# Optimization experiments

Hardware: AMD Instinct MI355X
Metric: run time of the kernel (lower is better)

The kernel has to match this reference:

```python
import jax, jax.numpy as jnp
import numpy as np

N = 50000      # total nodes
E = 800000     # total edges (before self-loops)
B = 512        # graphs in batch
H = 4          # attention heads
D = 64         # per-head dim (hidden 256 = H*D)
F_IN = 203     # node feature dim
HID = H * D
NEG_SLOPE = 0.2  # PyG GATConv LeakyReLU default
LN_EPS = 1e-5


def setup_inputs() -> dict:
    key = jax.random.key(0)
    ks = jax.random.split(key, 24)
    g = lambda k, shape, fan: (jax.random.normal(k, shape, jnp.float32) / np.sqrt(fan))
    inp = {
        "x": jax.random.normal(ks[0], (N, F_IN), jnp.float32),
        "edge_index": jax.random.randint(ks[1], (2, E), 0, N, jnp.int64),
        "edge_weight": jax.random.uniform(ks[2], (E,), jnp.float32),
        "batch": jnp.sort(jax.random.randint(ks[3], (N,), 0, B, jnp.int64)),
        # GAT layer 1 params
        "W1": g(ks[4], (HID, F_IN), F_IN),
        "a_s1": g(ks[5], (H, D), D),
        "a_d1": g(ks[6], (H, D), D),
        "a_e1": g(ks[7], (H, D), D),
        "We1": g(ks[8], (HID, 1), 1),
        "b1": jnp.zeros((HID,), jnp.float32),
        # GAT layer 2 params
        "W2": g(ks[9], (HID, HID), HID),
        "a_s2": g(ks[10], (H, D), D),
        "a_d2": g(ks[11], (H, D), D),
        "a_e2": g(ks[12], (H, D), D),
        "We2": g(ks[13], (HID, 1), 1),
        "b2": jnp.zeros((HID,), jnp.float32),
        # LayerNorms
        "ln1_g": jnp.ones((HID,), jnp.float32),
        "ln1_b": jnp.zeros((HID,), jnp.float32),
        "ln2_g": jnp.ones((HID,), jnp.float32),
        "ln2_b": jnp.zeros((HID,), jnp.float32),
    }
    return inp


def _gat(x, src, dst, e_attr, W, a_s, a_d, a_e, We, bias, n_nodes):
    # projected node features: [N, H, D]
    xp = (x @ W.T).reshape(n_nodes, H, D)
    alpha_src = jnp.einsum('nhd,hd->nh', xp, a_s)   # [N, H]
    alpha_dst = jnp.einsum('nhd,hd->nh', xp, a_d)   # [N, H]
    ep = (e_attr @ We.T).reshape(-1, H, D)          # [E', H, D]
    alpha_edge = jnp.einsum('ehd,hd->eh', ep, a_e)  # [E', H]
    logits = jax.nn.leaky_relu(alpha_src[src] + alpha_dst[dst] + alpha_edge, NEG_SLOPE)
    # segment softmax over incoming edges per destination node
    m = jax.ops.segment_max(logits, dst, num_segments=n_nodes)
    ex = jnp.exp(logits - m[dst])
    denom = jax.ops.segment_sum(ex, dst, num_segments=n_nodes)
    alpha = ex / denom[dst]                          # [E', H]
    msg = alpha[:, :, None] * xp[src]                # [E', H, D]
    out = jax.ops.segment_sum(msg, dst, num_segments=n_nodes)
    return out.reshape(n_nodes, HID) + bias


def _ln(x, g, b):
    mu = x.mean(-1, keepdims=True)
    var = ((x - mu) ** 2).mean(-1, keepdims=True)
    return (x - mu) * jax.lax.rsqrt(var + LN_EPS) * g + b


def reference(x, edge_index, edge_weight, batch,
              W1, a_s1, a_d1, a_e1, We1, b1,
              W2, a_s2, a_d2, a_e2, We2, b2,
              ln1_g, ln1_b, ln2_g, ln2_b):
    n = x.shape[0]
    # PyG GATConv add_self_loops=True, edge_attr fill_value='mean'
    loop = jnp.arange(n)
    src = jnp.concatenate([edge_index[0], loop])
    dst = jnp.concatenate([edge_index[1], loop])
    ew = jnp.concatenate([edge_weight, jnp.full((n,), edge_weight.mean(), edge_weight.dtype)])
    e_attr = ew[:, None]  # edge_dim = 1

    h = _gat(x, src, dst, e_attr, W1, a_s1, a_d1, a_e1, We1, b1, n)
    h = jax.nn.elu(_ln(h, ln1_g, ln1_b))  # dropout omitted (eval mode)
    h = _gat(h, src, dst, e_attr, W2, a_s2, a_d2, a_e2, We2, b2, n)
    h = jax.nn.elu(_ln(h, ln2_g, ln2_b))

    # global_mean_pool
    s = jax.ops.segment_sum(h, batch, num_segments=B)
    cnt = jax.ops.segment_sum(jnp.ones((n,), h.dtype), batch, num_segments=B)
    return s / jnp.maximum(cnt, 1.0)[:, None]
```

## Files before the change

### kernel.cpp

```cpp
#include <hip/hip_runtime.h>
#include <math.h>

#define HID 256
#define NEG_SLOPE 0.2f
#define LN_EPS 1e-5f

typedef __attribute__((ext_vector_type(4))) float f32x4;
typedef __attribute__((ext_vector_type(8))) short bf16x8;
typedef __attribute__((address_space(3))) unsigned char lds_b;
typedef const __attribute__((address_space(1))) unsigned char glob_b;

__device__ __forceinline__ float bf2f_lo(unsigned int u) {
    union { unsigned int i; float f; } c; c.i = u << 16; return c.f;
}
__device__ __forceinline__ float bf2f_hi(unsigned int u) {
    union { unsigned int i; float f; } c; c.i = u & 0xffff0000u; return c.f;
}
__device__ __forceinline__ float bf2f_u(unsigned short u) {
    union { unsigned int i; float f; } c; c.i = ((unsigned int)u) << 16; return c.f;
}
__device__ __forceinline__ unsigned short f2bf(float f) {
    union { float f; unsigned int i; } c; c.f = f;
    unsigned int i = c.i;
    return (unsigned short)((i + 0x7fffu + ((i >> 16) & 1u)) >> 16);
}

__global__ __launch_bounds__(256) void k_sum_hist(const float* __restrict__ ew, int E,
                                                  const int* __restrict__ ei, int N,
                                                  float* __restrict__ partials, int* __restrict__ deg) {
    int t = threadIdx.x;
    if (blockIdx.x < 256) {
        __shared__ float sdata[4];
        float v = 0.f;
        for (int i = blockIdx.x * 256 + t; i < E; i += 65536) v += ew[i];
        for (int o = 32; o; o >>= 1) v += __shfl_xor(v, o);
        if ((t & 63) == 0) sdata[t >> 6] = v;
        __syncthreads();
        if (t == 0) partials[blockIdx.x] = sdata[0] + sdata[1] + sdata[2] + sdata[3];
    } else {
        int e = (blockIdx.x - 256) * 256 + t;
        if (e >= E + N) return;
        int d = (e < E) ? ei[E + e] : (e - E);
        atomicAdd(&deg[d], 1);
    }
}

__global__ __launch_bounds__(256) void k_scanred_coeff(const int* __restrict__ deg, int N, int NB,
                                                       int* __restrict__ bsum,
                                                       const float* __restrict__ partials, float* __restrict__ sumw,
                                                       const float* __restrict__ We1, const float* __restrict__ ae1,
                                                       const float* __restrict__ We2, const float* __restrict__ ae2,
                                                       float* __restrict__ c1, float* __restrict__ c2) {
    int t = threadIdx.x;
    int b = blockIdx.x;
    if (b < NB) {
        __shared__ int sdata[4];
        int i = b * 256 + t;
        int v = (i < N) ? deg[i] : 0;
        for (int o = 32; o; o >>= 1) v += __shfl_xor(v, o);
        if ((t & 63) == 0) sdata[t >> 6] = v;
        __syncthreads();
        if (t == 0) bsum[b] = sdata[0] + sdata[1] + sdata[2] + sdata[3];
    } else if (b == NB) {
        __shared__ float sdata[4];
        float v = partials[t];
        for (int o = 32; o; o >>= 1) v += __shfl_xor(v, o);
        if ((t & 63) == 0) sdata[t >> 6] = v;
        __syncthreads();
        if (t == 0) *sumw = sdata[0] + sdata[1] + sdata[2] + sdata[3];
    } else {
        float v1 = We1[t] * ae1[t];
        float v2 = We2[t] * ae2[t];
        for (int o = 1; o < 64; o <<= 1) { v1 += __shfl_xor(v1, o); v2 += __shfl_xor(v2, o); }
        if ((t & 63) == 0) { c1[t >> 6] = v1; c2[t >> 6] = v2; }
    }
}

__global__ __launch_bounds__(256) void k_scan_apply(const int* __restrict__ deg, int N, int NB,
                                                    const int* __restrict__ bsum,
                                                    int* __restrict__ offs, int* __restrict__ cursor) {
    __shared__ int sm[256];
    __shared__ int sb[256];
    int t = threadIdx.x;
    int i = blockIdx.x * 256 + t;
    int v = (i < N) ? deg[i] : 0;
    int vb = (t < NB) ? bsum[t] : 0;
    sm[t] = v;
    sb[t] = vb;
    __syncthreads();
    for (int o = 1; o < 256; o <<= 1) {
        int tv = (t >= o) ? sm[t - o] : 0;
        int tb = (t >= o) ? sb[t - o] : 0;
        __syncthreads();
        sm[t] += tv;
        sb[t] += tb;
        __syncthreads();
    }
    int myb = bsum[blockIdx.x];
    int boff = sb[blockIdx.x] - myb;
    if (i < N) {
        int e = boff + sm[t] - v;
        offs[i] = e; cursor[i] = e;
        if (i == N - 1) offs[N] = boff + sm[t];
    }
}

__global__ __launch_bounds__(256) void k_scatter_cvt(const int* __restrict__ ei, int E, int N, int NS,
                                                     int* __restrict__ cursor, int* __restrict__ csr_eid,
                                                     const float* __restrict__ W1, const float* __restrict__ W2,
                                                     unsigned short* __restrict__ o1, unsigned short* __restrict__ o2, int K1,
                                                     const float* __restrict__ x, unsigned short* __restrict__ x16, int FIN) {
    int t = threadIdx.x;
    int b = blockIdx.x;
    if (b < NS) {
        int e = b * 256 + t;
        if (e >= E + N) return;
        int d = (e < E) ? ei[E + e] : (e - E);
        int pos = atomicAdd(&cursor[d], 1);
        csr_eid[pos] = e;
    } else if (b < NS + 512) {
        int wb = b - NS;
        const float* in = (wb < 256) ? W1 : W2;
        unsigned short* out = (wb < 256) ? o1 : o2;
        int K = (wb < 256) ? K1 : 256;
        int col = wb & 255;
        float v = (t < K) ? in[(size_t)col * K + t] : 0.f;
        int ks = t >> 5, j = (t >> 3) & 3, e = t & 7;
        out[ks * 8192 + j * 2048 + ((((col << 4) ^ (j << 4))) >> 1) + e] = f2bf(v);
    } else {
        int r = b - NS - 512;
        x16[(size_t)r * 256 + t] = (t < FIN) ? f2bf(x[(size_t)r * FIN + t]) : (unsigned short)0;
    }
}

__device__ __forceinline__ void gemm_dev(int bid,
    const unsigned short* __restrict__ A16, const unsigned short* __restrict__ Bt16, int M,
    const float* __restrict__ asf, const float* __restrict__ adf,
    unsigned short* __restrict__ C16, float* __restrict__ as_out, float* __restrict__ ad_out)
{
    __shared__ __align__(16) unsigned short Bsl[4 * 256 * 8];
    int t = threadIdx.x;
    int lane = t & 63, w = t >> 6;
    int row0 = bid << 5;
    int kg = lane >> 4, fr = lane & 15;

    int ar0 = row0 + fr;      if (ar0 >= M) ar0 = 0;
    int ar1 = row0 + 16 + fr; if (ar1 >= M) ar1 = 0;
    const unsigned short* ap0 = A16 + (size_t)ar0 * 256 + (kg << 3);
    const unsigned short* ap1 = A16 + (size_t)ar1 * 256 + (kg << 3);

    f32x4 acc[2][4];
#pragma unroll
    for (int i = 0; i < 2; i++)
#pragma unroll
        for (int j = 0; j < 4; j++) acc[i][j] = (f32x4){0.f, 0.f, 0.f, 0.f};

    for (int ks = 0; ks < 8; ks++) {
#pragma unroll
        for (int j = 0; j < 4; j++) {
            __builtin_amdgcn_global_load_lds(
                (glob_b*)(Bt16 + (size_t)ks * 8192 + j * 2048 + t * 8),
                (lds_b*)((char*)Bsl + j * 4096 + t * 16),
                16, 0, 0);
        }
        bf16x8 a0 = *(const bf16x8*)(ap0 + (ks << 5));
        bf16x8 a1 = *(const bf16x8*)(ap1 + (ks << 5));
        __syncthreads();
#pragma unroll
        for (int nf = 0; nf < 4; nf++) {
            int col = (w << 6) + (nf << 4) + fr;
            bf16x8 bv = *(const bf16x8*)((const char*)Bsl + (kg << 12) + (((col << 4)) ^ (kg << 4)));
            acc[0][nf] = __builtin_amdgcn_mfma_f32_16x16x32_bf16(a0, bv, acc[0][nf], 0, 0, 0);
            acc[1][nf] = __builtin_amdgcn_mfma_f32_16x16x32_bf16(a1, bv, acc[1][nf], 0, 0, 0);
        }
        __syncthreads();
    }

#pragma unroll
    for (int mf = 0; mf < 2; mf++)
#pragma unroll
        for (int j = 0; j < 4; j++) {
            int gr = row0 + mf * 16 + kg * 4 + j;
            if (gr < M) {
#pragma unroll
                for (int nf = 0; nf < 4; nf++)
                    C16[(size_t)gr * 256 + (w << 6) + (nf << 4) + fr] = f2bf(acc[mf][nf][j]);
            }
        }
    float asv[4], adv[4];
#pragma unroll
    for (int nf = 0; nf < 4; nf++) {
        int col = (w << 6) + (nf << 4) + fr;
        asv[nf] = asf[col]; adv[nf] = adf[col];
    }
#pragma unroll
    for (int mf = 0; mf < 2; mf++)
#pragma unroll
        for (int j = 0; j < 4; j++) {
            float ps = acc[mf][0][j] * asv[0] + acc[mf][1][j] * asv[1] + acc[mf][2][j] * asv[2] + acc[mf][3][j] * asv[3];
            float pd = acc[mf][0][j] * adv[0] + acc[mf][1][j] * adv[1] + acc[mf][2][j] * adv[2] + acc[mf][3][j] * adv[3];
#pragma unroll
            for (int o = 1; o < 16; o <<= 1) { ps += __shfl_xor(ps, o); pd += __shfl_xor(pd, o); }
            if (fr == 0) {
                int gr = row0 + mf * 16 + kg * 4 + j;
                if (gr < M) {
                    as_out[gr * 4 + w] = ps;
                    ad_out[gr * 4 + w] = pd;
                }
            }
        }
}

__device__ __forceinline__ void sort_gather_dev(int bid, const int* __restrict__ offs, int* __restrict__ eid,
                                                const int* __restrict__ ei, const float* __restrict__ ew,
                                                const float* __restrict__ sumw, int E, int N,
                                                int* __restrict__ csr_src, float* __restrict__ csr_w) {
    int lane = threadIdx.x & 63;
    int n = (bid << 2) + (threadIdx.x >> 6);
    if (n >= N) return;
    int s0 = offs[n];
    int d = offs[n + 1] - s0;
    if (d <= 0) return;
    if (d <= 64) {
        int key = (lane < d) ? eid[s0 + lane] : 0x7fffffff;
        int rank = 0;
        for (int j = 0; j < d; j++) {
            int kj = __shfl(key, j);
            rank += (kj < key) ? 1 : 0;
        }
        if (lane < d) {
            int s; float wv;
            if (key < E) { s = ei[key]; wv = ew[key]; }
            else         { s = key - E; wv = *sumw / (float)E; }
            csr_src[s0 + rank] = s;
            csr_w[s0 + rank] = wv;
        }
    } else {
        if (lane == 0) {
            for (int i = s0 + 1; i < s0 + d; i++) {
                int ke = eid[i];
                int j = i - 1;
                while (j >= s0 && eid[j] > ke) { eid[j + 1] = eid[j]; j--; }
                eid[j + 1] = ke;
            }
        }
        __builtin_amdgcn_wave_barrier();
        for (int i = lane; i < d; i += 64) {
            int e = eid[s0 + i];
            int s; float wv;
            if (e < E) { s = ei[e]; wv = ew[e]; }
            else       { s = e - E; wv = *sumw / (float)E; }
            csr_src[s0 + i] = s;
            csr_w[s0 + i] = wv;
        }
    }
}

__global__ __launch_bounds__(256) void k_gemm_sort(int MB,
    const unsigned short* __restrict__ A16, const unsigned short* __restrict__ Bt16, int M,
    const float* __restrict__ asf, const float* __restrict__ adf,
    unsigned short* __restrict__ C16, float* __restrict__ as_out, float* __restrict__ ad_out,
    const int* __restrict__ offs, int* __restrict__ eid,
    const int* __restrict__ ei, const float* __restrict__ ew,
    const float* __restrict__ sumw, int E,
    int* __restrict__ csr_src, float* __restrict__ csr_w) {
    if ((int)blockIdx.x < MB)
        gemm_dev(blockIdx.x, A16, Bt16, M, asf, adf, C16, as_out, ad_out);
    else
        sort_gather_dev(blockIdx.x - MB, offs, eid, ei, ew, sumw, E, M, csr_src, csr_w);
}

__global__ __launch_bounds__(256) void gemm_mfma(
    const unsigned short* __restrict__ A16, const unsigned short* __restrict__ Bt16, int M,
    const float* __restrict__ asf, const float* __restrict__ adf,
    unsigned short* __restrict__ C16, float* __restrict__ as_out, float* __restrict__ ad_out) {
    gemm_dev(blockIdx.x, A16, Bt16, M, asf, adf, C16, as_out, ad_out);
}

#define ACC8(u, q) do { \
    acc0 += (q) * bf2f_lo((u).x); acc1 += (q) * bf2f_hi((u).x); \
    acc2 += (q) * bf2f_lo((u).y); acc3 += (q) * bf2f_hi((u).y); \
    acc4 += (q) * bf2f_lo((u).z); acc5 += (q) * bf2f_hi((u).z); \
    acc6 += (q) * bf2f_lo((u).w); acc7 += (q) * bf2f_hi((u).w); } while (0)

__global__ __launch_bounds__(256) void gat_kernel(
    const unsigned short* __restrict__ xp16, const int* __restrict__ offs,
    const int* __restrict__ csr_src, const float* __restrict__ csr_w,
    const float* __restrict__ as_, const float* __restrict__ ad_,
    const float* __restrict__ cvec, const float* __restrict__ bias,
    const float* __restrict__ ln_g, const float* __restrict__ ln_b,
    int N, unsigned short* __restrict__ out16) {
    __shared__ float p_lds[4][256];
    __shared__ int   s_lds[4][64];
    int lane = threadIdx.x & 63;
    int wid = threadIdx.x >> 6;
    int n = (blockIdx.x << 2) + wid;
    if (n >= N) return;
    int start = offs[n], end = offs[n + 1];
    int e0 = lane >> 5;
    int colb = lane & 31;
    int hq2 = colb >> 3;
    const unsigned short* xbase = xp16 + (size_t)colb * 8;
    float4 adv = *(const float4*)(ad_ + (size_t)n * 4);
    float c0 = cvec[0], c1 = cvec[1], c2 = cvec[2], c3 = cvec[3];
    float m = -INFINITY, dn = 0.f;
    float acc0 = 0, acc1 = 0, acc2 = 0, acc3 = 0, acc4 = 0, acc5 = 0, acc6 = 0, acc7 = 0;

    for (int base = start; base < end; base += 64) {
        int idx = base + lane;
        bool act = idx < end;
        int s = act ? csr_src[idx] : 0;
        float w = act ? csr_w[idx] : 0.f;
        float4 av = *(const float4*)(as_ + (size_t)s * 4);
        float l0 = av.x + adv.x + w * c0; l0 = l0 >= 0.f ? l0 : NEG_SLOPE * l0;
        float l1 = av.y + adv.y + w * c1; l1 = l1 >= 0.f ? l1 : NEG_SLOPE * l1;
        float l2 = av.z + adv.z + w * c2; l2 = l2 >= 0.f ? l2 : NEG_SLOPE * l2;
        float l3 = av.w + adv.w + w * c3; l3 = l3 >= 0.f ? l3 : NEG_SLOPE * l3;
        float lm = fmaxf(fmaxf(l0, l1), fmaxf(l2, l3));
        if (!act) lm = -INFINITY;
        for (int o = 32; o; o >>= 1) lm = fmaxf(lm, __shfl_xor(lm, o));
        float nm = fmaxf(m, lm);
        float sc = __expf(m - nm);
        m = nm;
        dn *= sc;
        acc0 *= sc; acc1 *= sc; acc2 *= sc; acc3 *= sc;
        acc4 *= sc; acc5 *= sc; acc6 *= sc; acc7 *= sc;
        float p0 = act ? __expf(l0 - m) : 0.f;
        float p1 = act ? __expf(l1 - m) : 0.f;
        float p2 = act ? __expf(l2 - m) : 0.f;
        float p3 = act ? __expf(l3 - m) : 0.f;
        float4 pv = { p0, p1, p2, p3 };
        *(float4*)&p_lds[wid][lane << 2] = pv;
        s_lds[wid][lane] = s;
        int cnt = end - base; if (cnt > 64) cnt = 64;
        int k = 0;
        for (; k + 8 <= cnt; k += 8) {
            int i0 = k + e0, i1 = k + 2 + e0, i2 = k + 4 + e0, i3 = k + 6 + e0;
            int s0 = s_lds[wid][i0], s1 = s_lds[wid][i1], s2 = s_lds[wid][i2], s3 = s_lds[wid][i3];
            uint4 u0 = *(const uint4*)(xbase + (size_t)s0 * 256);
            uint4 u1 = *(const uint4*)(xbase + (size_t)s1 * 256);
            uint4 u2 = *(const uint4*)(xbase + (size_t)s2 * 256);
            uint4 u3 = *(const uint4*)(xbase + (size_t)s3 * 256);
            float q0 = p_lds[wid][(i0 << 2) + hq2];
            float q1 = p_lds[wid][(i1 << 2) + hq2];
            float q2 = p_lds[wid][(i2 << 2) + hq2];
            float q3 = p_lds[wid][(i3 << 2) + hq2];
            dn += q0 + q1 + q2 + q3;
            ACC8(u0, q0); ACC8(u1, q1); ACC8(u2, q2); ACC8(u3, q3);
        }
        for (; k < cnt; k += 2) {
            int i = k + e0;
            bool v = i < cnt;
            int si = s_lds[wid][v ? i : 0];
            float qi = v ? p_lds[wid][(i << 2) + hq2] : 0.f;
            uint4 u = *(const uint4*)(xbase + (size_t)si * 256);
            dn += qi;
            ACC8(u, qi);
        }
    }
    acc0 += __shfl_xor(acc0, 32); acc1 += __shfl_xor(acc1, 32);
    acc2 += __shfl_xor(acc2, 32); acc3 += __shfl_xor(acc3, 32);
    acc4 += __shfl_xor(acc4, 32); acc5 += __shfl_xor(acc5, 32);
    acc6 += __shfl_xor(acc6, 32); acc7 += __shfl_xor(acc7, 32);
    dn += __shfl_xor(dn, 32);
    float inv = 1.f / dn;
    int cb8 = colb << 3;
    float4 bA = *(const float4*)(bias + cb8);
    float4 bB = *(const float4*)(bias + cb8 + 4);
    float o0 = acc0 * inv + bA.x, o1 = acc1 * inv + bA.y, o2 = acc2 * inv + bA.z, o3 = acc3 * inv + bA.w;
    float o4 = acc4 * inv + bB.x, o5 = acc5 * inv + bB.y, o6 = acc6 * inv + bB.z, o7 = acc7 * inv + bB.w;
    float part = ((o0 + o1) + (o2 + o3)) + ((o4 + o5) + (o6 + o7));
    for (int o = 16; o; o >>= 1) part += __shfl_xor(part, o);
    float mu = part * (1.f / 256.f);
    float d0 = o0 - mu, d1 = o1 - mu, d2 = o2 - mu, d3 = o3 - mu;
    float d4 = o4 - mu, d5 = o5 - mu, d6 = o6 - mu, d7 = o7 - mu;
    float vpart = ((d0 * d0 + d1 * d1) + (d2 * d2 + d3 * d3)) + ((d4 * d4 + d5 * d5) + (d6 * d6 + d7 * d7));
    for (int o = 16; o; o >>= 1) vpart += __shfl_xor(vpart, o);
    float rstd = rsqrtf(vpart * (1.f / 256.f) + LN_EPS);
    float4 gA = *(const float4*)(ln_g + cb8), gB = *(const float4*)(ln_g + cb8 + 4);
    float4 eA = *(const float4*)(ln_b + cb8), eB = *(const float4*)(ln_b + cb8 + 4);
    float y0 = d0 * rstd * gA.x + eA.x; y0 = y0 > 0.f ? y0 : __expf(y0) - 1.f;
    float y1 = d1 * rstd * gA.y + eA.y; y1 = y1 > 0.f ? y1 : __expf(y1) - 1.f;
    float y2 = d2 * rstd * gA.z + eA.z; y2 = y2 > 0.f ? y2 : __expf(y2) - 1.f;
    float y3 = d3 * rstd * gA.w + eA.w; y3 = y3 > 0.f ? y3 : __expf(y3) - 1.f;
    float y4 = d4 * rstd * gB.x + eB.x; y4 = y4 > 0.f ? y4 : __expf(y4) - 1.f;
    float y5 = d5 * rstd * gB.y + eB.y; y5 = y5 > 0.f ? y5 : __expf(y5) - 1.f;
    float y6 = d6 * rstd * gB.z + eB.z; y6 = y6 > 0.f ? y6 : __expf(y6) - 1.f;
    float y7 = d7 * rstd * gB.w + eB.w; y7 = y7 > 0.f ? y7 : __expf(y7) - 1.f;
    if (lane < 32) {
        uint4 ov;
        ov.x = ((unsigned int)f2bf(y1) << 16) | f2bf(y0);
        ov.y = ((unsigned int)f2bf(y3) << 16) | f2bf(y2);
        ov.z = ((unsigned int)f2bf(y5) << 16) | f2bf(y4);
        ov.w = ((unsigned int)f2bf(y7) << 16) | f2bf(y6);
        *(uint4*)(out16 + (size_t)n * HID + cb8) = ov;
    }
}

__device__ __forceinline__ int lower_bound_i(const int* a, int n, int key) {
    int lo = 0, hi = n;
    while (lo < hi) { int mid = (lo + hi) >> 1; if (a[mid] < key) lo = mid + 1; else hi = mid; }
    return lo;
}

__global__ __launch_bounds__(256) void pool_kernel(const unsigned short* __restrict__ h, const int* __restrict__ batch,
                                                   int N, float* __restrict__ out) {
    int b = blockIdx.x;
    int lo = lower_bound_i(batch, N, b);
    int hi = lower_bound_i(batch, N, b + 1);
    float a0 = 0.f, a1 = 0.f, a2 = 0.f, a3 = 0.f;
    int n = lo;
    for (; n + 4 <= hi; n += 4) {
        a0 += bf2f_u(h[(size_t)(n + 0) * HID + threadIdx.x]);
        a1 += bf2f_u(h[(size_t)(n + 1) * HID + threadIdx.x]);
        a2 += bf2f_u(h[(size_t)(n + 2) * HID + threadIdx.x]);
        a3 += bf2f_u(h[(size_t)(n + 3) * HID + threadIdx.x]);
    }
    for (; n < hi; n++) a0 += bf2f_u(h[(size_t)n * HID + threadIdx.x]);
    float acc = (a0 + a1) + (a2 + a3);
    out[(size_t)b * HID + threadIdx.x] = acc / fmaxf((float)(hi - lo), 1.f);
}

extern "C" void kernel_launch(void* const* d_in, const int* in_sizes, int n_in,
                              void* d_out, int out_size, void* d_ws, size_t ws_size,
                              hipStream_t stream) {
    const float* x    = (const float*)d_in[0];
    const int*   ei   = (const int*)d_in[1];
    const float* ew   = (const float*)d_in[2];
    const int*   batch= (const int*)d_in[3];
    const float* W1   = (const float*)d_in[4];
    const float* as1  = (const float*)d_in[5];
    const float* ad1  = (const float*)d_in[6];
    const float* ae1  = (const float*)d_in[7];
    const float* We1  = (const float*)d_in[8];
    const float* b1   = (const float*)d_in[9];
    const float* W2   = (const float*)d_in[10];
    const float* as2  = (const float*)d_in[11];
    const float* ad2  = (const float*)d_in[12];
    const float* ae2  = (const float*)d_in[13];
    const float* We2  = (const float*)d_in[14];
    const float* b2   = (const float*)d_in[15];
    const float* ln1g = (const float*)d_in[16];
    const float* ln1b = (const float*)d_in[17];
    const float* ln2g = (const float*)d_in[18];
    const float* ln2b = (const float*)d_in[19];

    int N = in_sizes[3];
    int E = in_sizes[2];
    int FIN = in_sizes[0] / N;
    int EN = E + N;
    int B = out_size / HID;
    float* outp = (float*)d_out;
    int NB = (N + 255) / 256;
    int NS = (EN + 255) / 256;

    char* ws = (char*)d_ws;
    size_t off = 0;
    auto alloc = [&](size_t bytes) { void* p = ws + off; off = (off + bytes + 255) & ~(size_t)255; return p; };
    float* sumw    = (float*)alloc(4);
    int*   deg     = (int*)  alloc((size_t)N * 4);
    size_t zero_bytes = 256 + (size_t)N * 4;
    float* partials= (float*)alloc(256 * 4);
    int*   bsum    = (int*)  alloc(256 * 4);
    int*   offs    = (int*)  alloc((size_t)(N + 1) * 4);
    int*   cursor  = (int*)  alloc((size_t)N * 4);
    int*   csr_eid = (int*)  alloc((size_t)EN * 4);
    int*   csr_src = (int*)  alloc((size_t)EN * 4);
    float* csr_w   = (float*)alloc((size_t)EN * 4);
    float* asb     = (float*)alloc((size_t)N * 4 * 4);
    float* adb     = (float*)alloc((size_t)N * 4 * 4);
    float* cc      = (float*)alloc(64);
    unsigned short* w1_16 = (unsigned short*)alloc((size_t)HID * HID * 2);
    unsigned short* w2_16 = (unsigned short*)alloc((size_t)HID * HID * 2);
    unsigned short* x16   = (unsigned short*)alloc((size_t)N * HID * 2);
    unsigned short* xp16  = (unsigned short*)alloc((size_t)N * HID * 2);
    (void)ws_size; (void)n_in;

    int MB = (N + 31) / 32;

    (void)hipMemsetAsync(d_ws, 0, zero_bytes, stream);
    k_sum_hist<<<256 + NS, 256, 0, stream>>>(ew, E, ei, N, partials, deg);
    k_scanred_coeff<<<NB + 2, 256, 0, stream>>>(deg, N, NB, bsum, partials, sumw, We1, ae1, We2, ae2, cc, cc + 4);
    k_scan_apply<<<NB, 256, 0, stream>>>(deg, N, NB, bsum, offs, cursor);
    k_scatter_cvt<<<NS + 512 + N, 256, 0, stream>>>(ei, E, N, NS, cursor, csr_eid,
                                                    W1, W2, w1_16, w2_16, FIN, x, x16, FIN);
    k_gemm_sort<<<MB + (N + 3) / 4, 256, 0, stream>>>(MB, x16, w1_16, N, as1, ad1, xp16, asb, adb,
                                                      offs, csr_eid, ei, ew, sumw, E, csr_src, csr_w);
    gat_kernel<<<(N + 3) / 4, 256, 0, stream>>>(xp16, offs, csr_src, csr_w, asb, adb, cc, b1, ln1g, ln1b, N, x16);
    gemm_mfma<<<MB, 256, 0, stream>>>(x16, w2_16, N, as2, ad2, xp16, asb, adb);
    gat_kernel<<<(N + 3) / 4, 256, 0, stream>>>(xp16, offs, csr_src, csr_w, asb, adb, cc + 4, b2, ln2g, ln2b, N, x16);
    pool_kernel<<<B, 256, 0, stream>>>(x16, batch, N, outp);
}
```

Before: 352.4 us.

## Build CSR via fixed-capacity per-node bins in one pass, dropping scatter kernel

Replaces the histogram-then-scatter CSR build with a single pass that atomically appends each edge id into a fixed 128-slot bin per destination node, with overflow going to a global spill list. The separate scatter kernel and cursor array are removed, and the weight/feature conversions are folded into the same pre-kernel, saving one launch and a second pass over the edge list. The compaction step then reads the bins directly and sorts them. This adds a large sparsely written bins buffer and a slow serial spill scan for high-degree nodes.

```diff
diff --git a/kernel.cpp b/kernel.cpp
--- a/kernel.cpp
+++ b/kernel.cpp
@@ -4,6 +4,7 @@
 #define HID 256
 #define NEG_SLOPE 0.2f
 #define LN_EPS 1e-5f
+#define MAXDEG 128
 
 typedef __attribute__((ext_vector_type(4))) float f32x4;
 typedef __attribute__((ext_vector_type(8))) short bf16x8;
@@ -25,23 +26,48 @@
     return (unsigned short)((i + 0x7fffu + ((i >> 16) & 1u)) >> 16);
 }
 
-__global__ __launch_bounds__(256) void k_sum_hist(const float* __restrict__ ew, int E,
-                                                  const int* __restrict__ ei, int N,
-                                                  float* __restrict__ partials, int* __restrict__ deg) {
+__global__ __launch_bounds__(256) void k_pre(const float* __restrict__ ew, int E,
+                                             const int* __restrict__ ei, int N, int EN, int NH,
+                                             float* __restrict__ partials, int* __restrict__ bin_cnt,
+                                             int* __restrict__ bins, int* __restrict__ spill, int* __restrict__ spill_cnt,
+                                             const float* __restrict__ W1, const float* __restrict__ W2,
+                                             unsigned short* __restrict__ o1, unsigned short* __restrict__ o2, int K1,
+                                             const float* __restrict__ x, unsigned short* __restrict__ x16, int FIN) {
     int t = threadIdx.x;
-    if (blockIdx.x < 256) {
+    int b = blockIdx.x;
+    if (b < NH) {
+        int i = b * 1024 + t;
+#pragma unroll
+        for (int c = 0; c < 4; c++) {
+            int e = i + c * 256;
+            if (e < EN) {
+                int d = (e < E) ? ei[E + e] : (e - E);
+                int pos = atomicAdd(&bin_cnt[d], 1);
+                if (pos < MAXDEG) bins[(size_t)d * MAXDEG + pos] = e;
+                else { int q = atomicAdd(spill_cnt, 1); spill[2 * q] = d; spill[2 * q + 1] = e; }
+            }
+        }
+    } else if (b < NH + 256) {
         __shared__ float sdata[4];
+        int sb = b - NH;
         float v = 0.f;
-        for (int i = blockIdx.x * 256 + t; i < E; i += 65536) v += ew[i];
+        for (int i = sb * 256 + t; i < E; i += 65536) v += ew[i];
         for (int o = 32; o; o >>= 1) v += __shfl_xor(v, o);
         if ((t & 63) == 0) sdata[t >> 6] = v;
         __syncthreads();
-        if (t == 0) partials[blockIdx.x] = sdata[0] + sdata[1] + sdata[2] + sdata[3];
+        if (t == 0) partials[sb] = sdata[0] + sdata[1] + sdata[2] + sdata[3];
+    } else if (b < NH + 256 + 512) {
+        int wb = b - NH - 256;
+        const float* in = (wb < 256) ? W1 : W2;
+        unsigned short* out = (wb < 256) ? o1 : o2;
+        int K = (wb < 256) ? K1 : 256;
+        int col = wb & 255;
+        float v = (t < K) ? in[(size_t)col * K + t] : 0.f;
+        int ks = t >> 5, j = (t >> 3) & 3, e = t & 7;
+        out[ks * 8192 + j * 2048 + ((((col << 4) ^ (j << 4))) >> 1) + e] = f2bf(v);
     } else {
-        int e = (blockIdx.x - 256) * 256 + t;
-        if (e >= E + N) return;
-        int d = (e < E) ? ei[E + e] : (e - E);
-        atomicAdd(&deg[d], 1);
+        int r = b - NH - 256 - 512;
+        x16[(size_t)r * 256 + t] = (t < FIN) ? f2bf(x[(size_t)r * FIN + t]) : (unsigned short)0;
     }
 }
 
@@ -77,8 +103,7 @@
 }
 
 __global__ __launch_bounds__(256) void k_scan_apply(const int* __restrict__ deg, int N, int NB,
-                                                    const int* __restrict__ bsum,
-                                                    int* __restrict__ offs, int* __restrict__ cursor) {
+                                                    const int* __restrict__ bsum, int* __restrict__ offs) {
     __shared__ int sm[256];
     __shared__ int sb[256];
     int t = threadIdx.x;
@@ -99,37 +124,8 @@
     int myb = bsum[blockIdx.x];
     int boff = sb[blockIdx.x] - myb;
     if (i < N) {
-        int e = boff + sm[t] - v;
-        offs[i] = e; cursor[i] = e;
+        offs[i] = boff + sm[t] - v;
         if (i == N - 1) offs[N] = boff + sm[t];
-    }
-}
-
-__global__ __launch_bounds__(256) void k_scatter_cvt(const int* __restrict__ ei, int E, int N, int NS,
-                                                     int* __restrict__ cursor, int* __restrict__ csr_eid,
-                                                     const float* __restrict__ W1, const float* __restrict__ W2,
-                                                     unsigned short* __restrict__ o1, unsigned short* __restrict__ o2, int K1,
-                                                     const float* __restrict__ x, unsigned short* __restrict__ x16, int FIN) {
-    int t = threadIdx.x;
-    int b = blockIdx.x;
-    if (b < NS) {
-        int e = b * 256 + t;
-        if (e >= E + N) return;
-        int d = (e < E) ? ei[E + e] : (e - E);
-        int pos = atomicAdd(&cursor[d], 1);
-        csr_eid[pos] = e;
-    } else if (b < NS + 512) {
-        int wb = b - NS;
-        const float* in = (wb < 256) ? W1 : W2;
-        unsigned short* out = (wb < 256) ? o1 : o2;
-        int K = (wb < 256) ? K1 : 256;
-        int col = wb & 255;
-        float v = (t < K) ? in[(size_t)col * K + t] : 0.f;
-        int ks = t >> 5, j = (t >> 3) & 3, e = t & 7;
-        out[ks * 8192 + j * 2048 + ((((col << 4) ^ (j << 4))) >> 1) + e] = f2bf(v);
-    } else {
-        int r = b - NS - 512;
-        x16[(size_t)r * 256 + t] = (t < FIN) ? f2bf(x[(size_t)r * FIN + t]) : (unsigned short)0;
     }
 }
 
@@ -211,10 +207,12 @@
         }
 }
 
-__device__ __forceinline__ void sort_gather_dev(int bid, const int* __restrict__ offs, int* __restrict__ eid,
-                                                const int* __restrict__ ei, const float* __restrict__ ew,
-                                                const float* __restrict__ sumw, int E, int N,
-                                                int* __restrict__ csr_src, float* __restrict__ csr_w) {
+__device__ __forceinline__ void compact_dev(int bid, const int* __restrict__ offs,
+                                            const int* __restrict__ bins,
+                                            const int* __restrict__ spill, const int* __restrict__ spill_cnt,
+                                            const int* __restrict__ ei, const float* __restrict__ ew,
+                                            const float* __restrict__ sumw, int E, int N,
+                                            int* __restrict__ csr_src, float* __restrict__ csr_w) {
     int lane = threadIdx.x & 63;
     int n = (bid << 2) + (threadIdx.x >> 6);
     if (n >= N) return;
@@ -222,7 +220,7 @@
     int d = offs[n + 1] - s0;
     if (d <= 0) return;
     if (d <= 64) {
-        int key = (lane < d) ? eid[s0 + lane] : 0x7fffffff;
+        int key = (lane < d) ? bins[(size_t)n * MAXDEG + lane] : 0x7fffffff;
         int rank = 0;
         for (int j = 0; j < d; j++) {
             int kj = __shfl(key, j);
@@ -237,16 +235,23 @@
         }
     } else {
         if (lane == 0) {
+            int m = (d < MAXDEG) ? d : MAXDEG;
+            for (int i = 0; i < m; i++) csr_src[s0 + i] = bins[(size_t)n * MAXDEG + i];
+            int cnt = m;
+            int st = *spill_cnt;
+            for (int k = 0; k < st; k++)
+                if (spill[2 * k] == n) csr_src[s0 + cnt++] = spill[2 * k + 1];
             for (int i = s0 + 1; i < s0 + d; i++) {
-                int ke = eid[i];
+                int ke = csr_src[i];
                 int j = i - 1;
-                while (j >= s0 && eid[j] > ke) { eid[j + 1] = eid[j]; j--; }
-                eid[j + 1] = ke;
+                while (j >= s0 && csr_src[j] > ke) { csr_src[j + 1] = csr_src[j]; j--; }
+                csr_src[j + 1] = ke;
             }
         }
+        __threadfence();
         __builtin_amdgcn_wave_barrier();
         for (int i = lane; i < d; i += 64) {
-            int e = eid[s0 + i];
+            int e = csr_src[s0 + i];
             int s; float wv;
             if (e < E) { s = ei[e]; wv = ew[e]; }
             else       { s = e - E; wv = *sumw / (float)E; }
@@ -260,14 +265,15 @@
     const unsigned short* __restrict__ A16, const unsigned short* __restrict__ Bt16, int M,
     const float* __restrict__ asf, const float* __restrict__ adf,
     unsigned short* __restrict__ C16, float* __restrict__ as_out, float* __restrict__ ad_out,
-    const int* __restrict__ offs, int* __restrict__ eid,
+    const int* __restrict__ offs, const int* __restrict__ bins,
+    const int* __restrict__ spill, const int* __restrict__ spill_cnt,
     const int* __restrict__ ei, const float* __restrict__ ew,
     const float* __restrict__ sumw, int E,
     int* __restrict__ csr_src, float* __restrict__ csr_w) {
     if ((int)blockIdx.x < MB)
         gemm_dev(blockIdx.x, A16, Bt16, M, asf, adf, C16, as_out, ad_out);
     else
-        sort_gather_dev(blockIdx.x - MB, offs, eid, ei, ew, sumw, E, M, csr_src, csr_w);
+        compact_dev(blockIdx.x - MB, offs, bins, spill, spill_cnt, ei, ew, sumw, E, M, csr_src, csr_w);
 }
 
 __global__ __launch_bounds__(256) void gemm_mfma(
@@ -452,19 +458,20 @@
     int B = out_size / HID;
     float* outp = (float*)d_out;
     int NB = (N + 255) / 256;
-    int NS = (EN + 255) / 256;
+    int NH = (EN + 1023) / 1024;
 
     char* ws = (char*)d_ws;
     size_t off = 0;
     auto alloc = [&](size_t bytes) { void* p = ws + off; off = (off + bytes + 255) & ~(size_t)255; return p; };
-    float* sumw    = (float*)alloc(4);
-    int*   deg     = (int*)  alloc((size_t)N * 4);
-    size_t zero_bytes = 256 + (size_t)N * 4;
+    float* sumw      = (float*)alloc(4);
+    int*   spill_cnt = (int*)  alloc(4);
+    int*   bin_cnt   = (int*)  alloc((size_t)N * 4);
+    size_t zero_bytes = 512 + (size_t)N * 4;
     float* partials= (float*)alloc(256 * 4);
     int*   bsum    = (int*)  alloc(256 * 4);
     int*   offs    = (int*)  alloc((size_t)(N + 1) * 4);
-    int*   cursor  = (int*)  alloc((size_t)N * 4);
-    int*   csr_eid = (int*)  alloc((size_t)EN * 4);
+    int*   bins    = (int*)  alloc((size_t)N * MAXDEG * 4);
+    int*   spill   = (int*)  alloc((size_t)EN * 2 * 4);
     int*   csr_src = (int*)  alloc((size_t)EN * 4);
     float* csr_w   = (float*)alloc((size_t)EN * 4);
     float* asb     = (float*)alloc((size_t)N * 4 * 4);
@@ -477,17 +484,18 @@
     (void)ws_size; (void)n_in;
 
     int MB = (N + 31) / 32;
+    int NC = (N + 3) / 4;
 
     (void)hipMemsetAsync(d_ws, 0, zero_bytes, stream);
-    k_sum_hist<<<256 + NS, 256, 0, stream>>>(ew, E, ei, N, partials, deg);
-    k_scanred_coeff<<<NB + 2, 256, 0, stream>>>(deg, N, NB, bsum, partials, sumw, We1, ae1, We2, ae2, cc, cc + 4);
-    k_scan_apply<<<NB, 256, 0, stream>>>(deg, N, NB, bsum, offs, cursor);
-    k_scatter_cvt<<<NS + 512 + N, 256, 0, stream>>>(ei, E, N, NS, cursor, csr_eid,
-                                                    W1, W2, w1_16, w2_16, FIN, x, x16, FIN);
-    k_gemm_sort<<<MB + (N + 3) / 4, 256, 0, stream>>>(MB, x16, w1_16, N, as1, ad1, xp16, asb, adb,
-                                                      offs, csr_eid, ei, ew, sumw, E, csr_src, csr_w);
-    gat_kernel<<<(N + 3) / 4, 256, 0, stream>>>(xp16, offs, csr_src, csr_w, asb, adb, cc, b1, ln1g, ln1b, N, x16);
+    k_pre<<<NH + 256 + 512 + N, 256, 0, stream>>>(ew, E, ei, N, EN, NH, partials, bin_cnt,
+                                                  bins, spill, spill_cnt,
+                                                  W1, W2, w1_16, w2_16, FIN, x, x16, FIN);
+    k_scanred_coeff<<<NB + 2, 256, 0, stream>>>(bin_cnt, N, NB, bsum, partials, sumw, We1, ae1, We2, ae2, cc, cc + 4);
+    k_scan_apply<<<NB, 256, 0, stream>>>(bin_cnt, N, NB, bsum, offs);
+    k_gemm_sort<<<MB + NC, 256, 0, stream>>>(MB, x16, w1_16, N, as1, ad1, xp16, asb, adb,
+                                             offs, bins, spill, spill_cnt, ei, ew, sumw, E, csr_src, csr_w);
+    gat_kernel<<<NC, 256, 0, stream>>>(xp16, offs, csr_src, csr_w, asb, adb, cc, b1, ln1g, ln1b, N, x16);
     gemm_mfma<<<MB, 256, 0, stream>>>(x16, w2_16, N, as2, ad2, xp16, asb, adb);
-    gat_kernel<<<(N + 3) / 4, 256, 0, stream>>>(xp16, offs, csr_src, csr_w, asb, adb, cc + 4, b2, ln2g, ln2b, N, x16);
+    gat_kernel<<<NC, 256, 0, stream>>>(xp16, offs, csr_src, csr_w, asb, adb, cc + 4, b2, ln2g, ln2b, N, x16);
     pool_kernel<<<B, 256, 0, stream>>>(x16, batch, N, outp);
 }
```

Measured after the change: 334.0 us. -5.2%, faster.
